# Kernel tuning notes

Hardware: AMD Instinct MI355X
Metric: run time of the kernel (lower is better)

Reference implementation:

```python
import jax, jax.numpy as jnp
import numpy as np

# Sizes (see shape_source): B=4, N1=8192, N2=4096, T=H1=15, E1=131072, E2=65536
# conv1: Fin=1, G1=64, K=12, H=15 (collapse_H=True -> temporal dim folds to 1)
# conv2: Fin=64, G2=32, K=12, H=1

def _cheb_norm(src, dst, w, n):
    # Scaled Laplacian with lambda_max=2 (PyG ChebConv sym norm): L_hat = -D^{-1/2} A D^{-1/2}
    deg = jax.ops.segment_sum(w, dst, num_segments=n)
    dinv = jnp.where(deg > 0, 1.0 / jnp.sqrt(deg), 0.0)
    return -w * dinv[src] * dinv[dst]

def _prop(h, src, dst, norm, n):
    # h: (N, D, B) -> (L_hat h): (N, D, B) via edge gather + segment-sum scatter
    return jax.ops.segment_sum(norm[:, None, None] * h[src], dst, num_segments=n)

def _cheb_time_conv(h, src, dst, norm, W, b, n):
    # Chebyshev recursion: T0=x, T1=L_hat x, Tk = 2 L_hat T_{k-1} - T_{k-2}
    # h: (N, D, B); W: (K, D, G); output (N, G, B). D folds temporal H and Fin.
    K = W.shape[0]
    y = jnp.einsum('ndb,dg->ngb', h, W[0])
    Tx_prev = h
    Tx_cur = _prop(h, src, dst, norm, n)
    y = y + jnp.einsum('ndb,dg->ngb', Tx_cur, W[1])
    for k in range(2, K):
        Tx_next = 2.0 * _prop(Tx_cur, src, dst, norm, n) - Tx_prev
        y = y + jnp.einsum('ndb,dg->ngb', Tx_next, W[k])
        Tx_prev, Tx_cur = Tx_cur, Tx_next
    return y + b[None, :, None]

def setup_inputs() -> dict:
    key = jax.random.key(0)
    ks = jax.random.split(key, 12)
    B, N1, N2, T = 4, 8192, 4096, 15
    E1, E2 = 131072, 65536
    K, G1, G2, C = 12, 64, 32, 6
    return {
        'x': jax.random.normal(ks[0], (B, N1, T), dtype=jnp.float32),
        'edge_index1': jax.random.randint(ks[1], (2, E1), 0, N1, dtype=jnp.int64),
        'edge_weight1': jax.random.uniform(ks[2], (E1,), dtype=jnp.float32),
        'edge_index2': jax.random.randint(ks[3], (2, E2), 0, N2, dtype=jnp.int64),
        'edge_weight2': jax.random.uniform(ks[4], (E2,), dtype=jnp.float32),
        'b_map': jax.random.normal(ks[5], (N2, N1), dtype=jnp.float32) * 0.02,
        'W1': jax.random.normal(ks[6], (K, T, 1, G1), dtype=jnp.float32) * 0.1,
        'b1': jax.random.normal(ks[7], (G1,), dtype=jnp.float32) * 0.1,
        'W2': jax.random.normal(ks[8], (K, 1, G1, G2), dtype=jnp.float32) * 0.05,
        'b2': jax.random.normal(ks[9], (G2,), dtype=jnp.float32) * 0.1,
        'fc_w': jax.random.normal(ks[10], (C, N2 * G2), dtype=jnp.float32) * 0.01,
        'fc_b': jax.random.normal(ks[11], (C,), dtype=jnp.float32) * 0.1,
    }

def reference(x, edge_index1, edge_weight1, edge_index2, edge_weight2,
              b_map, W1, b1, W2, b2, fc_w, fc_b):
    Bsz = x.shape[0]
    h = jnp.transpose(x, (1, 2, 0))                      # torch x.permute(1,2,0): (N1, T, B)
    n1 = h.shape[0]
    s1, d1 = edge_index1[0], edge_index1[1]
    norm1 = _cheb_norm(s1, d1, edge_weight1, n1)
    # conv1: collapse_H folds the whole T=H window -> (N1, G1, B)
    h = _cheb_time_conv(h, s1, d1, norm1, W1.reshape(W1.shape[0], -1, W1.shape[-1]), b1, n1)
    h = jax.nn.relu(h)
    # temporal/pooling mapping: torch.matmul(b, x.permute(2,3,0,1)).permute(2,3,0,1)
    h = jnp.einsum('mn,ngb->mgb', b_map, h)              # (N2, G1, B)
    n2 = h.shape[0]
    s2, d2 = edge_index2[0], edge_index2[1]
    norm2 = _cheb_norm(s2, d2, edge_weight2, n2)
    h = _cheb_time_conv(h, s2, d2, norm2, W2.reshape(W2.shape[0], -1, W2.shape[-1]), b2, n2)  # (N2, G2, B)
    # faithful torch .view(B, -1) on contiguous (N2, G2, 1, B)
    flat = jnp.reshape(h[:, :, None, :], (Bsz, -1))
    logits = flat @ fc_w.T + fc_b
    return jax.nn.log_softmax(logits, axis=1)
```

## Files before the change

kernel.cpp:

```cpp
#include <hip/hip_runtime.h>

#define NB   4
#define NN1  8192
#define TT   15
#define NN2  4096
#define KCH  12
#define GG1  64
#define GG2  32
#define NCLS 6
#define EE1  131072
#define EE2  65536

typedef __attribute__((ext_vector_type(8))) short bf16x8;
typedef __attribute__((ext_vector_type(4))) float f32x4;

__device__ inline short f2bf(float f) {
    unsigned u = __builtin_bit_cast(unsigned, f);
    u += 0x7FFFu + ((u >> 16) & 1u);
    return (short)(u >> 16);
}

__global__ void k_deg_hist(const int* __restrict__ ei, const float* __restrict__ w,
                           float* __restrict__ deg, int* __restrict__ cnt, int E) {
    int e = blockIdx.x * 256 + threadIdx.x;
    if (e < E) {
        int d = ei[E + e];
        atomicAdd(&deg[d], w[e]);
        atomicAdd(&cnt[d], 1);
    }
}

template <int N>
__global__ __launch_bounds__(1024) void k_scan(const int* __restrict__ cnt,
                                               int* __restrict__ offs, int* __restrict__ cur) {
    constexpr int PER = N / 1024;
    __shared__ int part[1024];
    int t = threadIdx.x;
    int loc[PER];
    int s = 0;
#pragma unroll
    for (int i = 0; i < PER; ++i) { loc[i] = s; s += cnt[t * PER + i]; }
    part[t] = s;
    __syncthreads();
    for (int off = 1; off < 1024; off <<= 1) {
        int v = (t >= off) ? part[t - off] : 0;
        __syncthreads();
        part[t] += v;
        __syncthreads();
    }
    int pre = t ? part[t - 1] : 0;
#pragma unroll
    for (int i = 0; i < PER; ++i) { int v = pre + loc[i]; offs[t * PER + i] = v; cur[t * PER + i] = v; }
    if (t == 1023) offs[N] = part[1023];
}

__global__ void k_fill(const int* __restrict__ ei, const float* __restrict__ w,
                       const float* __restrict__ deg, int* __restrict__ cur,
                       int* __restrict__ csrc, float* __restrict__ cnrm, int E) {
    int e = blockIdx.x * 256 + threadIdx.x;
    if (e < E) {
        int s = ei[e], d = ei[E + e];
        float ds = deg[s], dd = deg[d];
        float is = ds > 0.f ? 1.f / sqrtf(ds) : 0.f;
        float id = dd > 0.f ? 1.f / sqrtf(dd) : 0.f;
        int p = atomicAdd(&cur[d], 1);
        csrc[p] = s;
        cnrm[p] = -w[e] * is * id;
    }
}

__global__ void k_build_h0(const float* __restrict__ x, float* __restrict__ h0,
                           short* __restrict__ bf0) {
    int idx = blockIdx.x * 256 + threadIdx.x;
    if (idx < NN1 * 64) {
        int n = idx >> 6, r = idx & 63;
        float v = 0.f;
        if (r < 60) {
            int t = r >> 2, b = r & 3;
            v = x[(b * NN1 + n) * TT + t];
        }
        h0[idx] = v;
        bf0[(size_t)n * 768 + r] = f2bf(v);
    }
}

__global__ __launch_bounds__(64) void k_prop1(const float* __restrict__ hprev,
                                              const float* __restrict__ hprev2,
                                              float* __restrict__ hout, short* __restrict__ bfs,
                                              const int* __restrict__ offs,
                                              const int* __restrict__ csrc,
                                              const float* __restrict__ cnrm, int first) {
    int n = blockIdx.x;
    int lane = threadIdx.x;
    int es = lane >> 4, f4 = lane & 15;
    int e0 = offs[n], e1 = offs[n + 1];
    f32x4 acc = {0.f, 0.f, 0.f, 0.f};
    for (int e = e0 + es; e < e1; e += 4) {
        int s = csrc[e];
        float wv = cnrm[e];
        const float4 v = *(const float4*)(hprev + (size_t)s * 64 + f4 * 4);
        acc[0] = fmaf(wv, v.x, acc[0]);
        acc[1] = fmaf(wv, v.y, acc[1]);
        acc[2] = fmaf(wv, v.z, acc[2]);
        acc[3] = fmaf(wv, v.w, acc[3]);
    }
#pragma unroll
    for (int i = 0; i < 4; ++i) {
        acc[i] += __shfl_xor(acc[i], 16, 64);
        acc[i] += __shfl_xor(acc[i], 32, 64);
    }
    if (es == 0) {
        float4 t;
        if (first) {
            t = make_float4(acc[0], acc[1], acc[2], acc[3]);
        } else {
            float4 p = *(const float4*)(hprev2 + (size_t)n * 64 + f4 * 4);
            t = make_float4(2.f * acc[0] - p.x, 2.f * acc[1] - p.y,
                            2.f * acc[2] - p.z, 2.f * acc[3] - p.w);
        }
        *(float4*)(hout + (size_t)n * 64 + f4 * 4) = t;
        short4 s4;
        s4.x = f2bf(t.x); s4.y = f2bf(t.y); s4.z = f2bf(t.z); s4.w = f2bf(t.w);
        *(short4*)(bfs + (size_t)n * 768 + f4 * 4) = s4;
    }
}

__global__ __launch_bounds__(256) void k_prop2(const float* __restrict__ hprev,
                                               const float* __restrict__ hprev2,
                                               float* __restrict__ hout, short* __restrict__ bfs,
                                               const int* __restrict__ offs,
                                               const int* __restrict__ csrc,
                                               const float* __restrict__ cnrm, int first) {
    __shared__ f32x4 red[3][64];
    int n = blockIdx.x;
    int t = threadIdx.x;
    int w = t >> 6, lane = t & 63;
    int e0 = offs[n], e1 = offs[n + 1];
    f32x4 acc = {0.f, 0.f, 0.f, 0.f};
    for (int e = e0 + w; e < e1; e += 4) {
        int s = csrc[e];
        float wv = cnrm[e];
        const float4 v = *(const float4*)(hprev + (size_t)s * 256 + lane * 4);
        acc[0] = fmaf(wv, v.x, acc[0]);
        acc[1] = fmaf(wv, v.y, acc[1]);
        acc[2] = fmaf(wv, v.z, acc[2]);
        acc[3] = fmaf(wv, v.w, acc[3]);
    }
    if (w) red[w - 1][lane] = acc;
    __syncthreads();
    if (w == 0) {
        f32x4 s = acc + red[0][lane] + red[1][lane] + red[2][lane];
        float4 tt;
        if (first) {
            tt = make_float4(s[0], s[1], s[2], s[3]);
        } else {
            float4 p = *(const float4*)(hprev2 + (size_t)n * 256 + lane * 4);
            tt = make_float4(2.f * s[0] - p.x, 2.f * s[1] - p.y,
                             2.f * s[2] - p.z, 2.f * s[3] - p.w);
        }
        *(float4*)(hout + (size_t)n * 256 + lane * 4) = tt;
        short4 s4;
        s4.x = f2bf(tt.x); s4.y = f2bf(tt.y); s4.z = f2bf(tt.z); s4.w = f2bf(tt.w);
        *(short4*)(bfs + (size_t)n * 3072 + lane * 4) = s4;
    }
}

__global__ void k_w1p(const float* __restrict__ W1, short* __restrict__ W1p) {
    int idx = blockIdx.x * 256 + threadIdx.x;
    if (idx < 256 * 768) {
        int j = idx / 768, d = idx - j * 768;
        int g = j >> 2, b = j & 3;
        int k = d >> 6, r = d & 63, t = r >> 2, bp = r & 3;
        float v = (b == bp && t < TT) ? W1[k * (TT * GG1) + t * GG1 + g] : 0.f;
        W1p[idx] = f2bf(v);
    }
}
__global__ void k_w2p(const float* __restrict__ W2, short* __restrict__ W2p) {
    int idx = blockIdx.x * 256 + threadIdx.x;
    if (idx < 128 * 3072) {
        int j = idx / 3072, d = idx - j * 3072;
        int g = j >> 2, b = j & 3;
        int k = d >> 8, r = d & 255, G = r >> 2, bp = r & 3;
        float v = (b == bp) ? W2[k * (GG1 * GG2) + G * GG2 + g] : 0.f;
        W2p[idx] = f2bf(v);
    }
}

template <bool A_BF, bool B_BF, bool BIASRELU>
__global__ __launch_bounds__(256) void k_gemm(const void* __restrict__ Ap, int lda,
                                              const void* __restrict__ Bp, int ldb,
                                              const float* __restrict__ bias,
                                              float* __restrict__ Cf, int ldc,
                                              int Kc, size_t pstride) {
    __shared__ short As[64][64];
    __shared__ short Bs[64][64];
    int m0 = blockIdx.x * 64, j0 = blockIdx.y * 64;
    int z = blockIdx.z;
    int kbeg = z * Kc, kend = kbeg + Kc;
    float* C = Cf + (size_t)z * pstride;
    int t = threadIdx.x;
    int lane = t & 63, wid = t >> 6;
    int wm = (wid >> 1) * 32, wn = (wid & 1) * 32;
    int lc = lane & 15, kg = lane >> 4;
    int r4 = t >> 2, c4 = (t & 3) * 16;
    int bjq = t & 15, bk4 = (t >> 4) * 4;
    float bvbias = 0.f;
    if (BIASRELU) bvbias = bias[(j0 >> 2) + bjq];

    f32x4 acc[2][2] = {};

    for (int k0 = kbeg; k0 < kend; k0 += 64) {
        int swa = (r4 & 7) << 3;
        if (A_BF) {
            const short* ap = (const short*)Ap + (size_t)(m0 + r4) * lda + k0 + c4;
            bf16x8 v0 = *(const bf16x8*)ap;
            bf16x8 v1 = *(const bf16x8*)(ap + 8);
            *(bf16x8*)&As[r4][c4 ^ swa] = v0;
            *(bf16x8*)&As[r4][(c4 + 8) ^ swa] = v1;
        } else {
            const float* ap = (const float*)Ap + (size_t)(m0 + r4) * lda + k0 + (t & 3) * 4;
#pragma unroll
            for (int q = 0; q < 4; ++q) {
                float4 v = *(const float4*)(ap + 16 * q);
                short4 s;
                s.x = f2bf(v.x); s.y = f2bf(v.y); s.z = f2bf(v.z); s.w = f2bf(v.w);
                *(short4*)&As[r4][((t & 3) * 4 + 16 * q) ^ swa] = s;
            }
        }
        if (B_BF) {
            const short* bp = (const short*)Bp + (size_t)(j0 + r4) * ldb + k0 + c4;
            bf16x8 v0 = *(const bf16x8*)bp;
            bf16x8 v1 = *(const bf16x8*)(bp + 8);
            *(bf16x8*)&Bs[r4][c4 ^ swa] = v0;
            *(bf16x8*)&Bs[r4][(c4 + 8) ^ swa] = v1;
        } else {
            float4 bv[4];
#pragma unroll
            for (int r = 0; r < 4; ++r) {
                const float* bp = (const float*)Bp + (size_t)(k0 + bk4 + r) * ldb + j0 + bjq * 4;
                float4 v = *(const float4*)bp;
                if (BIASRELU) {
                    v.x = fmaxf(v.x + bvbias, 0.f);
                    v.y = fmaxf(v.y + bvbias, 0.f);
                    v.z = fmaxf(v.z + bvbias, 0.f);
                    v.w = fmaxf(v.w + bvbias, 0.f);
                }
                bv[r] = v;
            }
#pragma unroll
            for (int jj = 0; jj < 4; ++jj) {
                int row = bjq * 4 + jj;
                int sw = (row & 7) << 3;
                short4 s;
                s.x = f2bf(jj == 0 ? bv[0].x : jj == 1 ? bv[0].y : jj == 2 ? bv[0].z : bv[0].w);
                s.y = f2bf(jj == 0 ? bv[1].x : jj == 1 ? bv[1].y : jj == 2 ? bv[1].z : bv[1].w);
                s.z = f2bf(jj == 0 ? bv[2].x : jj == 1 ? bv[2].y : jj == 2 ? bv[2].z : bv[2].w);
                s.w = f2bf(jj == 0 ? bv[3].x : jj == 1 ? bv[3].y : jj == 2 ? bv[3].z : bv[3].w);
                *(short4*)&Bs[row][bk4 ^ sw] = s;
            }
        }
        __syncthreads();
#pragma unroll
        for (int ks = 0; ks < 2; ++ks) {
            int kk = ks * 32 + kg * 8;
            bf16x8 a[2], b[2];
#pragma unroll
            for (int mi = 0; mi < 2; ++mi) {
                int row = wm + mi * 16 + lc;
                a[mi] = *(bf16x8*)&As[row][kk ^ ((row & 7) << 3)];
            }
#pragma unroll
            for (int ni = 0; ni < 2; ++ni) {
                int row = wn + ni * 16 + lc;
                b[ni] = *(bf16x8*)&Bs[row][kk ^ ((row & 7) << 3)];
            }
#pragma unroll
            for (int mi = 0; mi < 2; ++mi)
#pragma unroll
                for (int ni = 0; ni < 2; ++ni)
                    acc[mi][ni] = __builtin_amdgcn_mfma_f32_16x16x32_bf16(a[mi], b[ni], acc[mi][ni], 0, 0, 0);
        }
        __syncthreads();
    }
#pragma unroll
    for (int mi = 0; mi < 2; ++mi)
#pragma unroll
        for (int ni = 0; ni < 2; ++ni)
#pragma unroll
            for (int r = 0; r < 4; ++r) {
                int row = m0 + wm + mi * 16 + kg * 4 + r, col = j0 + wn + ni * 16 + lc;
                C[(size_t)row * ldc + col] = acc[mi][ni][r];
            }
}

__global__ void k_red8(const float* __restrict__ part, float* __restrict__ Cf,
                       short* __restrict__ Cbf) {
    int i = blockIdx.x * 256 + threadIdx.x;
    if (i < NN2 * 64) {
        const float4* p = (const float4*)part + i;
        float4 s = p[0];
#pragma unroll
        for (int z = 1; z < 8; ++z) {
            float4 v = p[(size_t)z * NN2 * 64];
            s.x += v.x; s.y += v.y; s.z += v.z; s.w += v.w;
        }
        ((float4*)Cf)[i] = s;
        int n = i >> 6, col = (i & 63) * 4;
        short4 s4;
        s4.x = f2bf(s.x); s4.y = f2bf(s.y); s4.z = f2bf(s.z); s4.w = f2bf(s.w);
        *(short4*)(Cbf + (size_t)n * 3072 + col) = s4;
    }
}
__global__ void k_red4(const float* __restrict__ part, float* __restrict__ Cf) {
    int i = blockIdx.x * 256 + threadIdx.x;
    if (i < NN2 * 32) {
        const float4* p = (const float4*)part + i;
        float4 s = p[0];
#pragma unroll
        for (int z = 1; z < 4; ++z) {
            float4 v = p[(size_t)z * NN2 * 32];
            s.x += v.x; s.y += v.y; s.z += v.z; s.w += v.w;
        }
        ((float4*)Cf)[i] = s;
    }
}

__global__ __launch_bounds__(256) void k_fc(const float* __restrict__ y2, const float* __restrict__ b2,
                                            const float* __restrict__ fcw, float* __restrict__ logits) {
    int qc = blockIdx.x >> 4, ch = blockIdx.x & 15;
    int q = qc / NCLS, c = qc % NCLS;
    const float* yp = y2 + (size_t)q * 131072 + ch * 8192;
    const float* wp = fcw + (size_t)c * 131072 + ch * 8192;
    int t = threadIdx.x;
    float acc = 0.f;
#pragma unroll
    for (int it = 0; it < 8; ++it) {
        int o = it * 1024 + t * 4;
        float4 yv = *(const float4*)(yp + o);
        float4 wv = *(const float4*)(wp + o);
        float bg = b2[((ch * 8192 + o) >> 2) & 31];
        acc += (yv.x + bg) * wv.x + (yv.y + bg) * wv.y + (yv.z + bg) * wv.z + (yv.w + bg) * wv.w;
    }
#pragma unroll
    for (int o = 32; o; o >>= 1) acc += __shfl_down(acc, o, 64);
    __shared__ float red[4];
    if ((t & 63) == 0) red[t >> 6] = acc;
    __syncthreads();
    if (t == 0) atomicAdd(&logits[qc], red[0] + red[1] + red[2] + red[3]);
}

__global__ void k_lsm(const float* __restrict__ logits, const float* __restrict__ fcb,
                      float* __restrict__ out) {
    int q = threadIdx.x;
    if (q < NB) {
        float v[NCLS];
#pragma unroll
        for (int c = 0; c < NCLS; ++c) v[c] = logits[q * NCLS + c] + fcb[c];
        float m = -1e30f;
#pragma unroll
        for (int c = 0; c < NCLS; ++c) m = fmaxf(m, v[c]);
        float s = 0.f;
#pragma unroll
        for (int c = 0; c < NCLS; ++c) s += expf(v[c] - m);
        float lse = m + logf(s);
#pragma unroll
        for (int c = 0; c < NCLS; ++c) out[q * NCLS + c] = v[c] - lse;
    }
}

extern "C" void kernel_launch(void* const* d_in, const int* in_sizes, int n_in,
                              void* d_out, int out_size, void* d_ws, size_t ws_size,
                              hipStream_t stream) {
    const float* x    = (const float*)d_in[0];
    const int*   ei1  = (const int*)d_in[1];
    const float* ew1  = (const float*)d_in[2];
    const int*   ei2  = (const int*)d_in[3];
    const float* ew2  = (const float*)d_in[4];
    const float* bmap = (const float*)d_in[5];
    const float* W1   = (const float*)d_in[6];
    const float* b1   = (const float*)d_in[7];
    const float* W2   = (const float*)d_in[8];
    const float* b2   = (const float*)d_in[9];
    const float* fcw  = (const float*)d_in[10];
    const float* fcb  = (const float*)d_in[11];
    float* out = (float*)d_out;

    char* w = (char*)d_ws;
    size_t o = 0;
    auto alloc = [&](size_t bytes) {
        char* p = w + o;
        o += (bytes + 255) & ~(size_t)255;
        return p;
    };
    float* deg1  = (float*)alloc(NN1 * 4);
    float* deg2  = (float*)alloc(NN2 * 4);
    int*   cnt1  = (int*)alloc(NN1 * 4);
    int*   cnt2  = (int*)alloc(NN2 * 4);
    int*   offs1 = (int*)alloc((NN1 + 1) * 4);
    int*   offs2 = (int*)alloc((NN2 + 1) * 4);
    int*   cur1  = (int*)alloc(NN1 * 4);
    int*   cur2  = (int*)alloc(NN2 * 4);
    int*   csrc1 = (int*)alloc(EE1 * 4);
    float* cnrm1 = (float*)alloc(EE1 * 4);
    int*   csrc2 = (int*)alloc(EE2 * 4);
    float* cnrm2 = (float*)alloc(EE2 * 4);
    float* R1a = (float*)alloc(NN1 * 64 * 4);
    float* R1b = (float*)alloc(NN1 * 64 * 4);
    float* R1c = (float*)alloc(NN1 * 64 * 4);
    short* T1bf = (short*)alloc((size_t)NN1 * 768 * 2);
    float* y1  = (float*)alloc((size_t)NN1 * 256 * 4);
    float* R2a = (float*)alloc((size_t)NN2 * 256 * 4);
    float* R2b = (float*)alloc((size_t)NN2 * 256 * 4);
    float* R2c = (float*)alloc((size_t)NN2 * 256 * 4);
    short* T2bf = (short*)alloc((size_t)NN2 * 3072 * 2);
    float* y2  = (float*)alloc((size_t)NN2 * 128 * 4);
    short* W1p = (short*)alloc(256 * 768 * 2);
    short* W2p = (short*)alloc(128 * 3072 * 2);
    float* part8 = (float*)alloc((size_t)8 * NN2 * 256 * 4);
    float* part4 = (float*)alloc((size_t)4 * NN2 * 128 * 4);
    float* logits = (float*)alloc(256);

    hipMemsetAsync(deg1, 0, NN1 * 4, stream);
    hipMemsetAsync(deg2, 0, NN2 * 4, stream);
    hipMemsetAsync(cnt1, 0, NN1 * 4, stream);
    hipMemsetAsync(cnt2, 0, NN2 * 4, stream);
    hipMemsetAsync(logits, 0, 256, stream);
    k_deg_hist<<<EE1 / 256, 256, 0, stream>>>(ei1, ew1, deg1, cnt1, EE1);
    k_deg_hist<<<EE2 / 256, 256, 0, stream>>>(ei2, ew2, deg2, cnt2, EE2);
    k_scan<NN1><<<1, 1024, 0, stream>>>(cnt1, offs1, cur1);
    k_scan<NN2><<<1, 1024, 0, stream>>>(cnt2, offs2, cur2);
    k_fill<<<EE1 / 256, 256, 0, stream>>>(ei1, ew1, deg1, cur1, csrc1, cnrm1, EE1);
    k_fill<<<EE2 / 256, 256, 0, stream>>>(ei2, ew2, deg2, cur2, csrc2, cnrm2, EE2);

    k_w1p<<<(256 * 768) / 256, 256, 0, stream>>>(W1, W1p);
    k_w2p<<<(128 * 3072) / 256, 256, 0, stream>>>(W2, W2p);

    k_build_h0<<<(NN1 * 64) / 256, 256, 0, stream>>>(x, R1a, T1bf);
    {
        float *Tm1 = R1a, *Tm2 = nullptr, *fr = R1b, *spare = R1c;
        for (int k = 1; k < KCH; ++k) {
            k_prop1<<<NN1, 64, 0, stream>>>(Tm1, k == 1 ? Tm1 : Tm2, fr,
                                            T1bf + k * 64, offs1, csrc1, cnrm1, k == 1 ? 1 : 0);
            float* nf = (k == 1) ? spare : Tm2;
            Tm2 = Tm1; Tm1 = fr; fr = nf;
        }
    }
    {
        dim3 g(NN1 / 64, 256 / 64, 1);
        k_gemm<true, true, false><<<g, 256, 0, stream>>>(T1bf, 768, W1p, 768, nullptr,
                                                         y1, 256, 768, 0);
    }
    {
        dim3 g(NN2 / 64, 256 / 64, 8);
        k_gemm<false, false, true><<<g, 256, 0, stream>>>(bmap, NN1, y1, 256, b1,
                                                          part8, 256, 1024, (size_t)NN2 * 256);
        k_red8<<<(NN2 * 64 + 255) / 256, 256, 0, stream>>>(part8, R2a, T2bf);
    }
    {
        float *Tm1 = R2a, *Tm2 = nullptr, *fr = R2b, *spare = R2c;
        for (int k = 1; k < KCH; ++k) {
            k_prop2<<<NN2, 256, 0, stream>>>(Tm1, k == 1 ? Tm1 : Tm2, fr,
                                             T2bf + k * 256, offs2, csrc2, cnrm2, k == 1 ? 1 : 0);
            float* nf = (k == 1) ? spare : Tm2;
            Tm2 = Tm1; Tm1 = fr; fr = nf;
        }
    }
    {
        dim3 g(NN2 / 64, 128 / 64, 4);
        k_gemm<true, true, false><<<g, 256, 0, stream>>>(T2bf, 3072, W2p, 3072, nullptr,
                                                         part4, 128, 768, (size_t)NN2 * 128);
        k_red4<<<(NN2 * 32 + 255) / 256, 256, 0, stream>>>(part4, y2);
    }

    k_fc<<<NB * NCLS * 16, 256, 0, stream>>>(y2, b2, fcw, logits);
    k_lsm<<<1, 64, 0, stream>>>(logits, fcb, out);
}
```

Baseline: 616.0 us.

## Double-buffer GEMM LDS tiles and fuse bias-ReLU into transposed bf16 conv1 output

The GEMM kernel now uses two LDS buffers and prefetches the next K tile into registers while MFMAs run on the current one, so each iteration needs one barrier instead of two. The conv1 GEMM epilogue applies bias and ReLU and writes its output transposed as bf16. The b_map GEMM can then load its B operand with contiguous bf16 vector loads instead of strided fp32 loads with per-element conversion. This halves y1 traffic and removes the transposition work, at the cost of doubled LDS use, more registers, and 8-byte scattered stores in the epilogue.

```diff
diff --git a/kernel.cpp b/kernel.cpp
--- a/kernel.cpp
+++ b/kernel.cpp
@@ -186,80 +186,73 @@
     }
 }
 
-template <bool A_BF, bool B_BF, bool BIASRELU>
+template <bool A_BF, bool Y1EPI>
 __global__ __launch_bounds__(256) void k_gemm(const void* __restrict__ Ap, int lda,
-                                              const void* __restrict__ Bp, int ldb,
+                                              const short* __restrict__ Bp, int ldb,
                                               const float* __restrict__ bias,
                                               float* __restrict__ Cf, int ldc,
+                                              short* __restrict__ yT,
                                               int Kc, size_t pstride) {
-    __shared__ short As[64][64];
-    __shared__ short Bs[64][64];
+    __shared__ short As[2][64][64];
+    __shared__ short Bs[2][64][64];
     int m0 = blockIdx.x * 64, j0 = blockIdx.y * 64;
     int z = blockIdx.z;
-    int kbeg = z * Kc, kend = kbeg + Kc;
+    int kbeg = z * Kc;
     float* C = Cf + (size_t)z * pstride;
     int t = threadIdx.x;
     int lane = t & 63, wid = t >> 6;
     int wm = (wid >> 1) * 32, wn = (wid & 1) * 32;
     int lc = lane & 15, kg = lane >> 4;
     int r4 = t >> 2, c4 = (t & 3) * 16;
-    int bjq = t & 15, bk4 = (t >> 4) * 4;
-    float bvbias = 0.f;
-    if (BIASRELU) bvbias = bias[(j0 >> 2) + bjq];
+    int swa = (r4 & 7) << 3;
+
+    const float* apf = (const float*)Ap + (size_t)(m0 + r4) * lda + kbeg + (t & 3) * 4;
+    const short* apb = (const short*)Ap + (size_t)(m0 + r4) * lda + kbeg + c4;
+    const short* bp  = Bp + (size_t)(j0 + r4) * ldb + kbeg + c4;
+
+    float4 af0, af1, af2, af3;
+    bf16x8 ab0, ab1, bb0, bb1;
+
+    auto load_tile = [&](int k0) {
+        if (A_BF) {
+            ab0 = *(const bf16x8*)(apb + k0);
+            ab1 = *(const bf16x8*)(apb + k0 + 8);
+        } else {
+            af0 = *(const float4*)(apf + k0);
+            af1 = *(const float4*)(apf + k0 + 16);
+            af2 = *(const float4*)(apf + k0 + 32);
+            af3 = *(const float4*)(apf + k0 + 48);
+        }
+        bb0 = *(const bf16x8*)(bp + k0);
+        bb1 = *(const bf16x8*)(bp + k0 + 8);
+    };
+    auto write_tile = [&](int buf) {
+        if (A_BF) {
+            *(bf16x8*)&As[buf][r4][c4 ^ swa] = ab0;
+            *(bf16x8*)&As[buf][r4][(c4 + 8) ^ swa] = ab1;
+        } else {
+            short4 s;
+            s.x = f2bf(af0.x); s.y = f2bf(af0.y); s.z = f2bf(af0.z); s.w = f2bf(af0.w);
+            *(short4*)&As[buf][r4][((t & 3) * 4) ^ swa] = s;
+            s.x = f2bf(af1.x); s.y = f2bf(af1.y); s.z = f2bf(af1.z); s.w = f2bf(af1.w);
+            *(short4*)&As[buf][r4][((t & 3) * 4 + 16) ^ swa] = s;
+            s.x = f2bf(af2.x); s.y = f2bf(af2.y); s.z = f2bf(af2.z); s.w = f2bf(af2.w);
+            *(short4*)&As[buf][r4][((t & 3) * 4 + 32) ^ swa] = s;
+            s.x = f2bf(af3.x); s.y = f2bf(af3.y); s.z = f2bf(af3.z); s.w = f2bf(af3.w);
+            *(short4*)&As[buf][r4][((t & 3) * 4 + 48) ^ swa] = s;
+        }
+        *(bf16x8*)&Bs[buf][r4][c4 ^ swa] = bb0;
+        *(bf16x8*)&Bs[buf][r4][(c4 + 8) ^ swa] = bb1;
+    };
 
     f32x4 acc[2][2] = {};
-
-    for (int k0 = kbeg; k0 < kend; k0 += 64) {
-        int swa = (r4 & 7) << 3;
-        if (A_BF) {
-            const short* ap = (const short*)Ap + (size_t)(m0 + r4) * lda + k0 + c4;
-            bf16x8 v0 = *(const bf16x8*)ap;
-            bf16x8 v1 = *(const bf16x8*)(ap + 8);
-            *(bf16x8*)&As[r4][c4 ^ swa] = v0;
-            *(bf16x8*)&As[r4][(c4 + 8) ^ swa] = v1;
-        } else {
-            const float* ap = (const float*)Ap + (size_t)(m0 + r4) * lda + k0 + (t & 3) * 4;
-#pragma unroll
-            for (int q = 0; q < 4; ++q) {
-                float4 v = *(const float4*)(ap + 16 * q);
-                short4 s;
-                s.x = f2bf(v.x); s.y = f2bf(v.y); s.z = f2bf(v.z); s.w = f2bf(v.w);
-                *(short4*)&As[r4][((t & 3) * 4 + 16 * q) ^ swa] = s;
-            }
-        }
-        if (B_BF) {
-            const short* bp = (const short*)Bp + (size_t)(j0 + r4) * ldb + k0 + c4;
-            bf16x8 v0 = *(const bf16x8*)bp;
-            bf16x8 v1 = *(const bf16x8*)(bp + 8);
-            *(bf16x8*)&Bs[r4][c4 ^ swa] = v0;
-            *(bf16x8*)&Bs[r4][(c4 + 8) ^ swa] = v1;
-        } else {
-            float4 bv[4];
-#pragma unroll
-            for (int r = 0; r < 4; ++r) {
-                const float* bp = (const float*)Bp + (size_t)(k0 + bk4 + r) * ldb + j0 + bjq * 4;
-                float4 v = *(const float4*)bp;
-                if (BIASRELU) {
-                    v.x = fmaxf(v.x + bvbias, 0.f);
-                    v.y = fmaxf(v.y + bvbias, 0.f);
-                    v.z = fmaxf(v.z + bvbias, 0.f);
-                    v.w = fmaxf(v.w + bvbias, 0.f);
-                }
-                bv[r] = v;
-            }
-#pragma unroll
-            for (int jj = 0; jj < 4; ++jj) {
-                int row = bjq * 4 + jj;
-                int sw = (row & 7) << 3;
-                short4 s;
-                s.x = f2bf(jj == 0 ? bv[0].x : jj == 1 ? bv[0].y : jj == 2 ? bv[0].z : bv[0].w);
-                s.y = f2bf(jj == 0 ? bv[1].x : jj == 1 ? bv[1].y : jj == 2 ? bv[1].z : bv[1].w);
-                s.z = f2bf(jj == 0 ? bv[2].x : jj == 1 ? bv[2].y : jj == 2 ? bv[2].z : bv[2].w);
-                s.w = f2bf(jj == 0 ? bv[3].x : jj == 1 ? bv[3].y : jj == 2 ? bv[3].z : bv[3].w);
-                *(short4*)&Bs[row][bk4 ^ sw] = s;
-            }
-        }
-        __syncthreads();
+    const int NIT = Kc >> 6;
+    load_tile(0);
+    write_tile(0);
+    __syncthreads();
+    for (int it = 0; it < NIT; ++it) {
+        int cur = it & 1;
+        if (it + 1 < NIT) load_tile((it + 1) << 6);
 #pragma unroll
         for (int ks = 0; ks < 2; ++ks) {
             int kk = ks * 32 + kg * 8;
@@ -267,12 +260,12 @@
 #pragma unroll
             for (int mi = 0; mi < 2; ++mi) {
                 int row = wm + mi * 16 + lc;
-                a[mi] = *(bf16x8*)&As[row][kk ^ ((row & 7) << 3)];
+                a[mi] = *(bf16x8*)&As[cur][row][kk ^ ((row & 7) << 3)];
             }
 #pragma unroll
             for (int ni = 0; ni < 2; ++ni) {
                 int row = wn + ni * 16 + lc;
-                b[ni] = *(bf16x8*)&Bs[row][kk ^ ((row & 7) << 3)];
+                b[ni] = *(bf16x8*)&Bs[cur][row][kk ^ ((row & 7) << 3)];
             }
 #pragma unroll
             for (int mi = 0; mi < 2; ++mi)
@@ -280,17 +273,36 @@
                 for (int ni = 0; ni < 2; ++ni)
                     acc[mi][ni] = __builtin_amdgcn_mfma_f32_16x16x32_bf16(a[mi], b[ni], acc[mi][ni], 0, 0, 0);
         }
+        if (it + 1 < NIT) write_tile(cur ^ 1);
         __syncthreads();
     }
-#pragma unroll
-    for (int mi = 0; mi < 2; ++mi)
-#pragma unroll
-        for (int ni = 0; ni < 2; ++ni)
-#pragma unroll
-            for (int r = 0; r < 4; ++r) {
-                int row = m0 + wm + mi * 16 + kg * 4 + r, col = j0 + wn + ni * 16 + lc;
-                C[(size_t)row * ldc + col] = acc[mi][ni][r];
+
+    if (Y1EPI) {
+#pragma unroll
+        for (int mi = 0; mi < 2; ++mi)
+#pragma unroll
+            for (int ni = 0; ni < 2; ++ni) {
+                int col = j0 + wn + ni * 16 + lc;
+                float bb = bias[col >> 2];
+                int row = m0 + wm + mi * 16 + kg * 4;
+                short4 s;
+                s.x = f2bf(fmaxf(acc[mi][ni][0] + bb, 0.f));
+                s.y = f2bf(fmaxf(acc[mi][ni][1] + bb, 0.f));
+                s.z = f2bf(fmaxf(acc[mi][ni][2] + bb, 0.f));
+                s.w = f2bf(fmaxf(acc[mi][ni][3] + bb, 0.f));
+                *(short4*)(yT + (size_t)col * NN1 + row) = s;
             }
+    } else {
+#pragma unroll
+        for (int mi = 0; mi < 2; ++mi)
+#pragma unroll
+            for (int ni = 0; ni < 2; ++ni)
+#pragma unroll
+                for (int r = 0; r < 4; ++r) {
+                    int row = m0 + wm + mi * 16 + kg * 4 + r, col = j0 + wn + ni * 16 + lc;
+                    C[(size_t)row * ldc + col] = acc[mi][ni][r];
+                }
+    }
 }
 
 __global__ void k_red8(const float* __restrict__ part, float* __restrict__ Cf,
@@ -408,7 +420,7 @@
     float* R1b = (float*)alloc(NN1 * 64 * 4);
     float* R1c = (float*)alloc(NN1 * 64 * 4);
     short* T1bf = (short*)alloc((size_t)NN1 * 768 * 2);
-    float* y1  = (float*)alloc((size_t)NN1 * 256 * 4);
+    short* ybfT = (short*)alloc((size_t)256 * NN1 * 2);
     float* R2a = (float*)alloc((size_t)NN2 * 256 * 4);
     float* R2b = (float*)alloc((size_t)NN2 * 256 * 4);
     float* R2c = (float*)alloc((size_t)NN2 * 256 * 4);
@@ -447,13 +459,13 @@
     }
     {
         dim3 g(NN1 / 64, 256 / 64, 1);
-        k_gemm<true, true, false><<<g, 256, 0, stream>>>(T1bf, 768, W1p, 768, nullptr,
-                                                         y1, 256, 768, 0);
+        k_gemm<true, true><<<g, 256, 0, stream>>>(T1bf, 768, W1p, 768, b1,
+                                                  nullptr, 0, ybfT, 768, 0);
     }
     {
         dim3 g(NN2 / 64, 256 / 64, 8);
-        k_gemm<false, false, true><<<g, 256, 0, stream>>>(bmap, NN1, y1, 256, b1,
-                                                          part8, 256, 1024, (size_t)NN2 * 256);
+        k_gemm<false, false><<<g, 256, 0, stream>>>(bmap, NN1, ybfT, NN1, nullptr,
+                                                    part8, 256, nullptr, 1024, (size_t)NN2 * 256);
         k_red8<<<(NN2 * 64 + 255) / 256, 256, 0, stream>>>(part8, R2a, T2bf);
     }
     {
@@ -467,8 +479,8 @@
     }
     {
         dim3 g(NN2 / 64, 128 / 64, 4);
-        k_gemm<true, true, false><<<g, 256, 0, stream>>>(T2bf, 3072, W2p, 3072, nullptr,
-                                                         part4, 128, 768, (size_t)NN2 * 128);
+        k_gemm<true, false><<<g, 256, 0, stream>>>(T2bf, 3072, W2p, 3072, nullptr,
+                                                   part4, 128, nullptr, 768, (size_t)NN2 * 128);
         k_red4<<<(NN2 * 32 + 255) / 256, 256, 0, stream>>>(part4, y2);
     }
 
```

Result: faster. 555.3 us (-9.9%).
